# Optimization experiments

Hardware: AMD Instinct MI355X
Metric: run time of the kernel (lower is better)

Reference implementation:

```python
import jax, jax.numpy as jnp
import numpy as np

VOCAB = 100000
EMBED = 128
CONTEXT = 2  # context_size
B, L = 64, 2048


def setup_inputs() -> dict:
    key = jax.random.key(0)
    k1, k2 = jax.random.split(key)
    x = jax.random.randint(k1, (B, L), 0, VOCAB, dtype=jnp.int64)
    emb = jax.random.normal(k2, (VOCAB, EMBED), dtype=jnp.float32)
    return {"x": x, "emb": emb}


def reference(x, emb):
    # x: [B, L] int token ids; emb: [V, E]
    Bn, Ln = x.shape
    C = CONTEXT
    j = jnp.arange(Ln)  # positions
    # ordering matches torch: before = x[j-1], x[j-2], ..., x[j-C]; after = x[j+1..j+C]
    offsets = jnp.concatenate([-jnp.arange(1, C + 1), jnp.arange(1, C + 1)])  # [2C]
    idx = j[:, None] + offsets[None, :]  # [L, 2C]
    valid = (idx >= 0) & (idx < Ln)
    idx_c = jnp.clip(idx, 0, Ln - 1)
    tok = jnp.where(valid[None, :, :], x[:, idx_c], 0)  # [B, L, 2C]; OOB -> token 0
    # embedding gather then sum over the sequence dim (dim=1 in torch code)
    out = jnp.sum(emb[tok], axis=1)  # [B, 2C, E]
    return out
```

## Files before the change

kernel.cpp:

```cpp
#include <hip/hip_runtime.h>

#define EMBED  128
#define BATCH  64
#define SEQLEN 2048
#define NSLICE 4
#define SLICEF 32
#define BLOCK  1024
#define NROWG  (BLOCK / 8)
#define TOKPG  (SEQLEN / NROWG)

__device__ __forceinline__ float4 f4add(const float4 a, const float4 b) {
    return make_float4(a.x + b.x, a.y + b.y, a.z + b.z, a.w + b.w);
}
__device__ __forceinline__ float4 f4sub(const float4 a, const float4 b) {
    return make_float4(a.x - b.x, a.y - b.y, a.z - b.z, a.w - b.w);
}

__global__ __launch_bounds__(BLOCK) void cbow_onepass_kernel(
    const int* __restrict__ x, const float* __restrict__ emb,
    float* __restrict__ out) {
    const int b   = blockIdx.x >> 2;
    const int sl  = blockIdx.x & 3;
    const int tid = threadIdx.x;
    const int c   = tid & 7;
    const int r   = tid >> 3;

    __shared__ int    toks[SEQLEN];
    __shared__ float4 psum[NROWG][8];

    reinterpret_cast<int2*>(toks)[tid] =
        reinterpret_cast<const int2*>(x + b * SEQLEN)[tid];
    __syncthreads();

    const float* embs = emb + sl * SLICEF + c * 4;
    float4 a0 = make_float4(0.f, 0.f, 0.f, 0.f);
    float4 a1 = a0, a2 = a0, a3 = a0;
#pragma unroll
    for (int it = 0; it < TOKPG; it += 4) {
        const float4 v0 = *reinterpret_cast<const float4*>(
            embs + (size_t)toks[r + NROWG * (it + 0)] * EMBED);
        const float4 v1 = *reinterpret_cast<const float4*>(
            embs + (size_t)toks[r + NROWG * (it + 1)] * EMBED);
        const float4 v2 = *reinterpret_cast<const float4*>(
            embs + (size_t)toks[r + NROWG * (it + 2)] * EMBED);
        const float4 v3 = *reinterpret_cast<const float4*>(
            embs + (size_t)toks[r + NROWG * (it + 3)] * EMBED);
        a0 = f4add(a0, v0);
        a1 = f4add(a1, v1);
        a2 = f4add(a2, v2);
        a3 = f4add(a3, v3);
    }
    psum[r][c] = f4add(f4add(a0, a1), f4add(a2, a3));
    __syncthreads();

#pragma unroll
    for (int s = NROWG / 2; s >= 1; s >>= 1) {
        if (r < s) psum[r][c] = f4add(psum[r][c], psum[r + s][c]);
        __syncthreads();
    }

    if (tid < 32) {
        const int o = tid >> 3;
        const float4 S = psum[0][c];
        const int t0  = toks[0];
        const int t1  = toks[1];
        const int tl2 = toks[SEQLEN - 2];
        const int tl1 = toks[SEQLEN - 1];
        const float4 e0  = *reinterpret_cast<const float4*>(embs);
        const float4 v0  = *reinterpret_cast<const float4*>(embs + (size_t)t0  * EMBED);
        const float4 v1  = *reinterpret_cast<const float4*>(embs + (size_t)t1  * EMBED);
        const float4 vl2 = *reinterpret_cast<const float4*>(embs + (size_t)tl2 * EMBED);
        const float4 vl1 = *reinterpret_cast<const float4*>(embs + (size_t)tl1 * EMBED);

        float4 res = f4add(S, e0);
        if (o == 0) {
            res = f4sub(res, vl1);
        } else if (o == 1) {
            res = f4add(f4sub(f4sub(res, vl1), vl2), e0);
        } else if (o == 2) {
            res = f4sub(res, v0);
        } else {
            res = f4add(f4sub(f4sub(res, v0), v1), e0);
        }

        *reinterpret_cast<float4*>(
            out + ((size_t)b * 4 + o) * EMBED + sl * SLICEF + c * 4) = res;
    }
}

extern "C" void kernel_launch(void* const* d_in, const int* in_sizes, int n_in,
                              void* d_out, int out_size, void* d_ws, size_t ws_size,
                              hipStream_t stream) {
    const int*   x   = (const int*)d_in[0];
    const float* emb = (const float*)d_in[1];
    float*       out = (float*)d_out;

    cbow_onepass_kernel<<<dim3(BATCH * NSLICE), dim3(BLOCK), 0, stream>>>(
        x, emb, out);
}
```

Baseline: 15.31 us.

## Use wavefront shuffles for reduction, prefetch edge embeddings, remap block-to-batch order

Replaces the seven-step shared-memory tree reduction, which had a barrier per step, with intra-wavefront xor shuffles followed by a single cross-wave shared-memory step, leaving only two barriers. The edge-correction embedding rows are now loaded at kernel start so their latency overlaps the main gather instead of sitting at the tail. Block indices are also remapped so neighbouring blocks cover adjacent batch rows within the same slice, which may change L2 locality. Each lane does more shuffle work in exchange for fewer barriers.

```diff
diff --git a/kernel.cpp b/kernel.cpp
--- a/kernel.cpp
+++ b/kernel.cpp
@@ -15,24 +15,47 @@
 __device__ __forceinline__ float4 f4sub(const float4 a, const float4 b) {
     return make_float4(a.x - b.x, a.y - b.y, a.z - b.z, a.w - b.w);
 }
+__device__ __forceinline__ float4 f4shfl_xor(const float4 v, int mask) {
+    return make_float4(__shfl_xor(v.x, mask), __shfl_xor(v.y, mask),
+                       __shfl_xor(v.z, mask), __shfl_xor(v.w, mask));
+}
 
 __global__ __launch_bounds__(BLOCK) void cbow_onepass_kernel(
     const int* __restrict__ x, const float* __restrict__ emb,
     float* __restrict__ out) {
-    const int b   = blockIdx.x >> 2;
-    const int sl  = blockIdx.x & 3;
+    const int idx = blockIdx.x;
+    const int sl  = (idx & 7) >> 1;
+    const int b   = ((idx >> 3) << 1) | (idx & 1);
     const int tid = threadIdx.x;
     const int c   = tid & 7;
     const int r   = tid >> 3;
+    const int w   = tid >> 6;
+    const int ln  = tid & 63;
+
+    const float* embs = emb + sl * SLICEF + c * 4;
+
+    float4 e0v, v0v, v1v, vl2v, vl1v;
+    if (tid < 32) {
+        const int ec  = tid & 7;
+        const float* embe = emb + sl * SLICEF + ec * 4;
+        const int t0  = x[b * SEQLEN + 0];
+        const int t1  = x[b * SEQLEN + 1];
+        const int tl2 = x[b * SEQLEN + SEQLEN - 2];
+        const int tl1 = x[b * SEQLEN + SEQLEN - 1];
+        e0v  = *reinterpret_cast<const float4*>(embe);
+        v0v  = *reinterpret_cast<const float4*>(embe + (size_t)t0  * EMBED);
+        v1v  = *reinterpret_cast<const float4*>(embe + (size_t)t1  * EMBED);
+        vl2v = *reinterpret_cast<const float4*>(embe + (size_t)tl2 * EMBED);
+        vl1v = *reinterpret_cast<const float4*>(embe + (size_t)tl1 * EMBED);
+    }
 
     __shared__ int    toks[SEQLEN];
-    __shared__ float4 psum[NROWG][8];
+    __shared__ float4 psum[16][8];
 
     reinterpret_cast<int2*>(toks)[tid] =
         reinterpret_cast<const int2*>(x + b * SEQLEN)[tid];
     __syncthreads();
 
-    const float* embs = emb + sl * SLICEF + c * 4;
     float4 a0 = make_float4(0.f, 0.f, 0.f, 0.f);
     float4 a1 = a0, a2 = a0, a3 = a0;
 #pragma unroll
@@ -50,39 +73,37 @@
         a2 = f4add(a2, v2);
         a3 = f4add(a3, v3);
     }
-    psum[r][c] = f4add(f4add(a0, a1), f4add(a2, a3));
+    float4 acc = f4add(f4add(a0, a1), f4add(a2, a3));
+
+    acc = f4add(acc, f4shfl_xor(acc, 8));
+    acc = f4add(acc, f4shfl_xor(acc, 16));
+    acc = f4add(acc, f4shfl_xor(acc, 32));
+    if (ln < 8) psum[w][c] = acc;
     __syncthreads();
 
-#pragma unroll
-    for (int s = NROWG / 2; s >= 1; s >>= 1) {
-        if (r < s) psum[r][c] = f4add(psum[r][c], psum[r + s][c]);
-        __syncthreads();
+    if (w == 0) {
+        const int g = ln >> 3;
+        float4 t = f4add(psum[g][c], psum[g + 8][c]);
+        t = f4add(t, f4shfl_xor(t, 8));
+        t = f4add(t, f4shfl_xor(t, 16));
+        t = f4add(t, f4shfl_xor(t, 32));
+        if (ln < 8) psum[0][c] = t;
     }
+    __syncthreads();
 
     if (tid < 32) {
         const int o = tid >> 3;
         const float4 S = psum[0][c];
-        const int t0  = toks[0];
-        const int t1  = toks[1];
-        const int tl2 = toks[SEQLEN - 2];
-        const int tl1 = toks[SEQLEN - 1];
-        const float4 e0  = *reinterpret_cast<const float4*>(embs);
-        const float4 v0  = *reinterpret_cast<const float4*>(embs + (size_t)t0  * EMBED);
-        const float4 v1  = *reinterpret_cast<const float4*>(embs + (size_t)t1  * EMBED);
-        const float4 vl2 = *reinterpret_cast<const float4*>(embs + (size_t)tl2 * EMBED);
-        const float4 vl1 = *reinterpret_cast<const float4*>(embs + (size_t)tl1 * EMBED);
-
-        float4 res = f4add(S, e0);
+        float4 res = f4add(S, e0v);
         if (o == 0) {
-            res = f4sub(res, vl1);
+            res = f4sub(res, vl1v);
         } else if (o == 1) {
-            res = f4add(f4sub(f4sub(res, vl1), vl2), e0);
+            res = f4add(f4sub(f4sub(res, vl1v), vl2v), e0v);
         } else if (o == 2) {
-            res = f4sub(res, v0);
+            res = f4sub(res, v0v);
         } else {
-            res = f4add(f4sub(f4sub(res, v0), v1), e0);
+            res = f4add(f4sub(f4sub(res, v0v), v1v), e0v);
         }
-
         *reinterpret_cast<float4*>(
             out + ((size_t)b * 4 + o) * EMBED + sl * SLICEF + c * 4) = res;
     }
```

New measurement: 14.21 us. -7.2%, faster.
